# Kernel tuning notes

Hardware: AMD Instinct MI355X
Metric: run time of the kernel (lower is better)

Reference implementation:

```python
import jax, jax.numpy as jnp
import numpy as np

BATCH = 131072
STATE_DIM = 64
CONTROL_DIM = 16
HIDDEN = 256
ALPHA = 0.1
MAX_ITERS = 200
TOL = 0.01
TRACKED_ITERS = 5
U_MIN, U_MAX = -1.0, 1.0


def setup_inputs() -> dict:
    key = jax.random.key(0)
    ks = jax.random.split(key, 8)
    def w(k, shape, fan_in):
        return (jax.random.normal(k, shape, jnp.float32) / np.float32(np.sqrt(fan_in)))
    x = jax.random.normal(ks[0], (BATCH, STATE_DIM), jnp.float32)
    t = jax.random.uniform(ks[1], (1,), jnp.float32)
    W1 = w(ks[2], (STATE_DIM + 1, HIDDEN), STATE_DIM + 1)
    b1 = jnp.zeros((HIDDEN,), jnp.float32)
    W2 = w(ks[3], (HIDDEN, HIDDEN), HIDDEN)
    b2 = jnp.zeros((HIDDEN,), jnp.float32)
    W3 = w(ks[4], (HIDDEN, STATE_DIM), HIDDEN)
    b3 = jnp.zeros((STATE_DIM,), jnp.float32)
    Bmat = w(ks[5], (STATE_DIM, CONTROL_DIM), STATE_DIM)  # oc_problem dynamics matrix
    return {"x": x, "t": t, "W1": W1, "b1": b1, "W2": W2, "b2": b2,
            "W3": W3, "b3": b3, "Bmat": Bmat}


def _p_net(t, x, W1, b1, W2, b2, W3, b3):
    # DefaultPNet: pad x with scalar t, then 3-layer ReLU MLP -> p in [B, state_dim]
    n = x.shape[0]
    tcol = jnp.broadcast_to(t.reshape(1, 1).astype(x.dtype), (n, 1))
    zt = jnp.concatenate([x, tcol], axis=1)
    h = jax.nn.relu(zt @ W1 + b1)
    h = jax.nn.relu(h @ W2 + b2)
    return h @ W3 + b3


def reference(x, t, W1, b1, W2, b2, W3, b3, Bmat):
    # grad_H_u(t,x,u,p) = u + p @ Bmat  (LQ Hamiltonian); p independent of u,
    # so p is computed once (same math as recomputing it every iteration).
    p = _p_net(t, x, W1, b1, W2, b2, W3, b3)          # [B, state_dim]
    pB = p @ Bmat                                      # [B, control_dim]
    clamp = lambda u: jnp.clip(u, U_MIN, U_MAX)
    T = lambda u, pb: u - ALPHA * (u + pb)

    u0 = jnp.zeros((x.shape[0], CONTROL_DIM), x.dtype)
    pB_ng = jax.lax.stop_gradient(pB)

    def cond(st):
        _, i, res = st
        return (res >= TOL) & (i < MAX_ITERS)

    def body(st):
        u, i, _ = st
        u_new = clamp(T(u, pB_ng))
        res = jnp.max(jnp.linalg.norm(u_new - u, axis=1)) / ALPHA
        return (u_new, i + 1, res)

    u_fp, _, _ = jax.lax.while_loop(cond, body, (u0, jnp.int32(0), jnp.float32(jnp.inf)))

    # training path: tracked_iters differentiable refinement steps + final T
    u = jax.lax.stop_gradient(u_fp)
    for _ in range(TRACKED_ITERS + 1):
        u = clamp(T(u, pB))
    return u
```

## Files before the change

kernel.cpp:

```cpp
#include <hip/hip_runtime.h>


typedef __bf16 bf16;
typedef __bf16 bf16x8 __attribute__((ext_vector_type(8)));
typedef __bf16 bf16x4 __attribute__((ext_vector_type(4)));
typedef float  f32x4  __attribute__((ext_vector_type(4)));

#define HID    256
#define SDIM   64
#define CDIM   16
#define BM     64
#define GRID   512
#define ITERS  4

#define OFF_W2P 0
#define OFF_W3P 131072
#define OFF_W1P 139264
#define OFF_B1E 172032
#define OFF_B3B 173056

#define MFMA(a, b, c) __builtin_amdgcn_mfma_f32_16x16x32_bf16(a, b, c, 0, 0, 0)

__device__ __forceinline__ int sh_idx(int row, int h) {
  return (row << 8) + ((((h >> 3) ^ row) & 7) << 3) + (h & 7) + ((h >> 6) << 6);
}
__device__ __forceinline__ int sx_idx(int row, int k) {
  return (row << 6) + ((((k >> 3) ^ row) & 7) << 3) + (k & 7);
}

__global__ __launch_bounds__(512)
void oc_pack(const float* __restrict__ t,  const float* __restrict__ W1,
             const float* __restrict__ b1, const float* __restrict__ W2,
             const float* __restrict__ W3, const float* __restrict__ b3,
             const float* __restrict__ Bmat, char* __restrict__ ws) {
  const int gid = blockIdx.x * 512 + threadIdx.x;
  if (gid < 8192) {
    const int lane = gid & 63, tt = gid >> 6;
    const int nt = tt & 15, kt = tt >> 4;
    const int m = nt * 16 + (lane & 15);
    const int k0 = kt * 32 + ((lane >> 4) << 3);
    bf16x8 v;
#pragma unroll
    for (int j = 0; j < 8; ++j) v[j] = (bf16)W2[(k0 + j) * HID + m];
    *(bf16x8*)((bf16*)(ws + OFF_W2P) + (size_t)gid * 8) = v;
  } else if (gid < 8704) {
    const int e = gid - 8192, kt = e >> 6, fl = e & 63;
    const int r0 = kt * 32 + ((fl >> 4) << 3);
    const int c  = fl & 15;
    float aw[8];
#pragma unroll
    for (int j = 0; j < 8; ++j) aw[j] = 0.f;
    for (int m = 0; m < SDIM; ++m) {
      const float bm = Bmat[m * CDIM + c];
#pragma unroll
      for (int j = 0; j < 8; ++j) aw[j] = fmaf(W3[(r0 + j) * SDIM + m], bm, aw[j]);
    }
    bf16x8 v;
#pragma unroll
    for (int j = 0; j < 8; ++j) v[j] = (bf16)aw[j];
    *(bf16x8*)((bf16*)(ws + OFF_W3P) + (size_t)e * 8) = v;
  } else if (gid < 10752) {
    const int e = gid - 8704;
    const int lane = e & 63, tt = e >> 6;
    const int nt = tt & 15, kt = tt >> 4;
    const int m = nt * 16 + (lane & 15);
    const int k0 = kt * 32 + ((lane >> 4) << 3);
    bf16x8 v;
#pragma unroll
    for (int j = 0; j < 8; ++j) v[j] = (bf16)W1[(k0 + j) * HID + m];
    *(bf16x8*)((bf16*)(ws + OFF_W1P) + (size_t)e * 8) = v;
  } else if (gid < 11008) {
    const int h = gid - 10752;
    ((float*)(ws + OFF_B1E))[h] = b1[h] + t[0] * W1[SDIM * HID + h];
  } else if (gid < 11024) {
    const int c = gid - 11008;
    float s = 0.f;
    for (int m = 0; m < SDIM; ++m) s = fmaf(b3[m], Bmat[m * CDIM + c], s);
    ((float*)(ws + OFF_B3B))[c] = s;
  }
}

__global__ __launch_bounds__(512, 2)
void oc_main(const float* __restrict__ x, const float* __restrict__ b2,
             const char* __restrict__ ws, float* __restrict__ out) {
  __shared__ bf16 sH1[BM * 256];
  __shared__ bf16 sH2[BM * 256];
  __shared__ bf16 sX [BM * 64];
  const int tid  = threadIdx.x;
  const int wave = tid >> 6, lane = tid & 63;
  const int q    = lane >> 4, l = lane & 15;

  const bf16* W2p = (const bf16*)(ws + OFF_W2P);
  const bf16* W3p = (const bf16*)(ws + OFF_W3P);
  const bf16* W1p = (const bf16*)(ws + OFF_W1P);

  {
    const float* xp = x + (size_t)blockIdx.x * BM * SDIM;
#pragma unroll
    for (int i = 0; i < 2; ++i) {
      const int e = i * 512 + tid;
      const int r = e >> 4, k4 = (e & 15) * 4;
      const float4 v = *(const float4*)(xp + r * SDIM + k4);
      bf16x4 w = {(bf16)v.x, (bf16)v.y, (bf16)v.z, (bf16)v.w};
      *(bf16x4*)(&sX[sx_idx(r, k4)]) = w;
    }
  }
  __syncthreads();

  f32x4 acc[2][4];

  for (int it = 0; it < ITERS; ++it) {
    const int tile = blockIdx.x + it * GRID;

#pragma unroll
    for (int mt = 0; mt < 2; ++mt) {
      const float4 v1 = *(const float4*)((const float*)(ws + OFF_B1E) + 32 * wave + 16 * mt + 4 * q);
      const f32x4 bv = {v1.x, v1.y, v1.z, v1.w};
#pragma unroll
      for (int nt = 0; nt < 4; ++nt) acc[mt][nt] = bv;
    }
#pragma unroll
    for (int kt = 0; kt < 2; ++kt) {
      const bf16x8 w1a = *(const bf16x8*)(W1p + ((size_t)(kt * 16 + 2 * wave    ) * 64 + lane) * 8);
      const bf16x8 w1b = *(const bf16x8*)(W1p + ((size_t)(kt * 16 + 2 * wave + 1) * 64 + lane) * 8);
#pragma unroll
      for (int nt = 0; nt < 4; ++nt) {
        const bf16x8 b = *(const bf16x8*)(&sX[sx_idx(16 * nt + l, 32 * kt + 8 * q)]);
        acc[0][nt] = MFMA(w1a, b, acc[0][nt]);
        acc[1][nt] = MFMA(w1b, b, acc[1][nt]);
      }
    }
#pragma unroll
    for (int mt = 0; mt < 2; ++mt) {
      const int h0 = 32 * wave + 16 * mt + 4 * q;
#pragma unroll
      for (int nt = 0; nt < 4; ++nt) {
        bf16x4 v;
#pragma unroll
        for (int r = 0; r < 4; ++r) v[r] = (bf16)fmaxf(acc[mt][nt][r], 0.f);
        *(bf16x4*)(&sH1[sh_idx(16 * nt + l, h0)]) = v;
      }
    }
    __syncthreads();

#pragma unroll
    for (int mt = 0; mt < 2; ++mt) {
      const float4 v2 = *(const float4*)(b2 + 32 * wave + 16 * mt + 4 * q);
      const f32x4 bv = {v2.x, v2.y, v2.z, v2.w};
#pragma unroll
      for (int nt = 0; nt < 4; ++nt) acc[mt][nt] = bv;
    }
#pragma unroll
    for (int kt = 0; kt < 8; ++kt) {
      const bf16x8 w2a = *(const bf16x8*)(W2p + ((size_t)(kt * 16 + 2 * wave    ) * 64 + lane) * 8);
      const bf16x8 w2b = *(const bf16x8*)(W2p + ((size_t)(kt * 16 + 2 * wave + 1) * 64 + lane) * 8);
#pragma unroll
      for (int nt = 0; nt < 4; ++nt) {
        const bf16x8 b = *(const bf16x8*)(&sH1[sh_idx(16 * nt + l, 32 * kt + 8 * q)]);
        acc[0][nt] = MFMA(w2a, b, acc[0][nt]);
        acc[1][nt] = MFMA(w2b, b, acc[1][nt]);
      }
    }
    __syncthreads();

#pragma unroll
    for (int mt = 0; mt < 2; ++mt) {
      const int h0 = 32 * wave + 16 * mt + 4 * q;
#pragma unroll
      for (int nt = 0; nt < 4; ++nt) {
        bf16x4 hi, lo;
#pragma unroll
        for (int r = 0; r < 4; ++r) {
          const float v = fmaxf(acc[mt][nt][r], 0.f);
          const bf16 h = (bf16)v;
          hi[r] = h;
          lo[r] = (bf16)(v - (float)h);
        }
        const int idx = sh_idx(16 * nt + l, h0);
        *(bf16x4*)(&sH2[idx]) = hi;
        *(bf16x4*)(&sH1[idx]) = lo;
      }
    }
    __syncthreads();

    if (wave < 4) {
      const float4 v3 = *(const float4*)((const float*)(ws + OFF_B3B) + 4 * q);
      f32x4 a3 = {v3.x, v3.y, v3.z, v3.w};
      const int row = 16 * wave + l;
#pragma unroll
      for (int kt = 0; kt < 8; ++kt) {
        const bf16x8 w3 = *(const bf16x8*)(W3p + ((size_t)kt * 64 + lane) * 8);
        const int idx = sh_idx(row, 32 * kt + 8 * q);
        const bf16x8 bh = *(const bf16x8*)(&sH2[idx]);
        const bf16x8 bl = *(const bf16x8*)(&sH1[idx]);
        a3 = MFMA(w3, bh, a3);
        a3 = MFMA(w3, bl, a3);
      }
      f32x4 o;
#pragma unroll
      for (int r = 0; r < 4; ++r)
        o[r] = fminf(fmaxf(-a3[r], -1.f), 1.f);
      *(float4*)(&out[((size_t)tile * BM + row) * CDIM + 4 * q]) = *(float4*)&o;
    } else if (it + 1 < ITERS) {
      const float* xp = x + (size_t)(tile + GRID) * BM * SDIM;
      const int tid2 = tid - 256;
#pragma unroll
      for (int i = 0; i < 4; ++i) {
        const int e = i * 256 + tid2;
        const int r = e >> 4, k4 = (e & 15) * 4;
        const float4 v = *(const float4*)(xp + r * SDIM + k4);
        bf16x4 w = {(bf16)v.x, (bf16)v.y, (bf16)v.z, (bf16)v.w};
        *(bf16x4*)(&sX[sx_idx(r, k4)]) = w;
      }
    }
    __syncthreads();
  }
}

extern "C" void kernel_launch(void* const* d_in, const int* in_sizes, int n_in,
                              void* d_out, int out_size, void* d_ws, size_t ws_size,
                              hipStream_t stream) {
  const float* x    = (const float*)d_in[0];
  const float* t    = (const float*)d_in[1];
  const float* W1   = (const float*)d_in[2];
  const float* b1   = (const float*)d_in[3];
  const float* W2   = (const float*)d_in[4];
  const float* b2   = (const float*)d_in[5];
  const float* W3   = (const float*)d_in[6];
  const float* b3   = (const float*)d_in[7];
  const float* Bmat = (const float*)d_in[8];
  float* out = (float*)d_out;
  char*  ws  = (char*)d_ws;

  hipLaunchKernelGGL(oc_pack, dim3(22), dim3(512), 0, stream,
                     t, W1, b1, W2, W3, b3, Bmat, ws);
  hipLaunchKernelGGL(oc_main, dim3(GRID), dim3(512), 0, stream,
                     x, b2, ws, out);
}
```

Measured before the change: 126.4 us.

## Double row tile to 128 with 1024-thread blocks sharing weight fragments

Each block now handles 128 rows with 16 waves. Waves are split into 8 hidden-column groups and 2 row halves, so one set of W1/W2 register fragments is spread across more rows per block. The grid is halved to 256 blocks, and the W2 and W3 loops drop to unroll-by-2, presumably to limit register pressure at 1024 threads. LDS per block doubles to about 144KB, which likely allows only one block per CU. The grid now covers fewer CUs than the device has (256 blocks).

```diff
diff --git a/kernel.cpp b/kernel.cpp
--- a/kernel.cpp
+++ b/kernel.cpp
@@ -9,8 +9,8 @@
 #define HID    256
 #define SDIM   64
 #define CDIM   16
-#define BM     64
-#define GRID   512
+#define BM     128
+#define GRID   256
 #define ITERS  4
 
 #define OFF_W2P 0
@@ -80,7 +80,7 @@
   }
 }
 
-__global__ __launch_bounds__(512, 2)
+__global__ __launch_bounds__(1024)
 void oc_main(const float* __restrict__ x, const float* __restrict__ b2,
              const char* __restrict__ ws, float* __restrict__ out) {
   __shared__ bf16 sH1[BM * 256];
@@ -89,6 +89,8 @@
   const int tid  = threadIdx.x;
   const int wave = tid >> 6, lane = tid & 63;
   const int q    = lane >> 4, l = lane & 15;
+  const int mg   = wave >> 1;
+  const int ng   = wave & 1;
 
   const bf16* W2p = (const bf16*)(ws + OFF_W2P);
   const bf16* W3p = (const bf16*)(ws + OFF_W3P);
@@ -98,7 +100,7 @@
     const float* xp = x + (size_t)blockIdx.x * BM * SDIM;
 #pragma unroll
     for (int i = 0; i < 2; ++i) {
-      const int e = i * 512 + tid;
+      const int e = i * 1024 + tid;
       const int r = e >> 4, k4 = (e & 15) * 4;
       const float4 v = *(const float4*)(xp + r * SDIM + k4);
       bf16x4 w = {(bf16)v.x, (bf16)v.y, (bf16)v.z, (bf16)v.w};
@@ -114,49 +116,49 @@
 
 #pragma unroll
     for (int mt = 0; mt < 2; ++mt) {
-      const float4 v1 = *(const float4*)((const float*)(ws + OFF_B1E) + 32 * wave + 16 * mt + 4 * q);
+      const float4 v1 = *(const float4*)((const float*)(ws + OFF_B1E) + 32 * mg + 16 * mt + 4 * q);
       const f32x4 bv = {v1.x, v1.y, v1.z, v1.w};
 #pragma unroll
       for (int nt = 0; nt < 4; ++nt) acc[mt][nt] = bv;
     }
 #pragma unroll
     for (int kt = 0; kt < 2; ++kt) {
-      const bf16x8 w1a = *(const bf16x8*)(W1p + ((size_t)(kt * 16 + 2 * wave    ) * 64 + lane) * 8);
-      const bf16x8 w1b = *(const bf16x8*)(W1p + ((size_t)(kt * 16 + 2 * wave + 1) * 64 + lane) * 8);
-#pragma unroll
-      for (int nt = 0; nt < 4; ++nt) {
-        const bf16x8 b = *(const bf16x8*)(&sX[sx_idx(16 * nt + l, 32 * kt + 8 * q)]);
+      const bf16x8 w1a = *(const bf16x8*)(W1p + ((size_t)(kt * 16 + 2 * mg    ) * 64 + lane) * 8);
+      const bf16x8 w1b = *(const bf16x8*)(W1p + ((size_t)(kt * 16 + 2 * mg + 1) * 64 + lane) * 8);
+#pragma unroll
+      for (int nt = 0; nt < 4; ++nt) {
+        const bf16x8 b = *(const bf16x8*)(&sX[sx_idx(64 * ng + 16 * nt + l, 32 * kt + 8 * q)]);
         acc[0][nt] = MFMA(w1a, b, acc[0][nt]);
         acc[1][nt] = MFMA(w1b, b, acc[1][nt]);
       }
     }
 #pragma unroll
     for (int mt = 0; mt < 2; ++mt) {
-      const int h0 = 32 * wave + 16 * mt + 4 * q;
+      const int h0 = 32 * mg + 16 * mt + 4 * q;
 #pragma unroll
       for (int nt = 0; nt < 4; ++nt) {
         bf16x4 v;
 #pragma unroll
         for (int r = 0; r < 4; ++r) v[r] = (bf16)fmaxf(acc[mt][nt][r], 0.f);
-        *(bf16x4*)(&sH1[sh_idx(16 * nt + l, h0)]) = v;
-      }
-    }
-    __syncthreads();
-
-#pragma unroll
-    for (int mt = 0; mt < 2; ++mt) {
-      const float4 v2 = *(const float4*)(b2 + 32 * wave + 16 * mt + 4 * q);
+        *(bf16x4*)(&sH1[sh_idx(64 * ng + 16 * nt + l, h0)]) = v;
+      }
+    }
+    __syncthreads();
+
+#pragma unroll
+    for (int mt = 0; mt < 2; ++mt) {
+      const float4 v2 = *(const float4*)(b2 + 32 * mg + 16 * mt + 4 * q);
       const f32x4 bv = {v2.x, v2.y, v2.z, v2.w};
 #pragma unroll
       for (int nt = 0; nt < 4; ++nt) acc[mt][nt] = bv;
     }
-#pragma unroll
+#pragma unroll 2
     for (int kt = 0; kt < 8; ++kt) {
-      const bf16x8 w2a = *(const bf16x8*)(W2p + ((size_t)(kt * 16 + 2 * wave    ) * 64 + lane) * 8);
-      const bf16x8 w2b = *(const bf16x8*)(W2p + ((size_t)(kt * 16 + 2 * wave + 1) * 64 + lane) * 8);
-#pragma unroll
-      for (int nt = 0; nt < 4; ++nt) {
-        const bf16x8 b = *(const bf16x8*)(&sH1[sh_idx(16 * nt + l, 32 * kt + 8 * q)]);
+      const bf16x8 w2a = *(const bf16x8*)(W2p + ((size_t)(kt * 16 + 2 * mg    ) * 64 + lane) * 8);
+      const bf16x8 w2b = *(const bf16x8*)(W2p + ((size_t)(kt * 16 + 2 * mg + 1) * 64 + lane) * 8);
+#pragma unroll
+      for (int nt = 0; nt < 4; ++nt) {
+        const bf16x8 b = *(const bf16x8*)(&sH1[sh_idx(64 * ng + 16 * nt + l, 32 * kt + 8 * q)]);
         acc[0][nt] = MFMA(w2a, b, acc[0][nt]);
         acc[1][nt] = MFMA(w2b, b, acc[1][nt]);
       }
@@ -165,7 +167,7 @@
 
 #pragma unroll
     for (int mt = 0; mt < 2; ++mt) {
-      const int h0 = 32 * wave + 16 * mt + 4 * q;
+      const int h0 = 32 * mg + 16 * mt + 4 * q;
 #pragma unroll
       for (int nt = 0; nt < 4; ++nt) {
         bf16x4 hi, lo;
@@ -176,18 +178,18 @@
           hi[r] = h;
           lo[r] = (bf16)(v - (float)h);
         }
-        const int idx = sh_idx(16 * nt + l, h0);
+        const int idx = sh_idx(64 * ng + 16 * nt + l, h0);
         *(bf16x4*)(&sH2[idx]) = hi;
         *(bf16x4*)(&sH1[idx]) = lo;
       }
     }
     __syncthreads();
 
-    if (wave < 4) {
+    if (wave < 8) {
       const float4 v3 = *(const float4*)((const float*)(ws + OFF_B3B) + 4 * q);
       f32x4 a3 = {v3.x, v3.y, v3.z, v3.w};
       const int row = 16 * wave + l;
-#pragma unroll
+#pragma unroll 2
       for (int kt = 0; kt < 8; ++kt) {
         const bf16x8 w3 = *(const bf16x8*)(W3p + ((size_t)kt * 64 + lane) * 8);
         const int idx = sh_idx(row, 32 * kt + 8 * q);
@@ -203,10 +205,10 @@
       *(float4*)(&out[((size_t)tile * BM + row) * CDIM + 4 * q]) = *(float4*)&o;
     } else if (it + 1 < ITERS) {
       const float* xp = x + (size_t)(tile + GRID) * BM * SDIM;
-      const int tid2 = tid - 256;
+      const int tid2 = tid - 512;
 #pragma unroll
       for (int i = 0; i < 4; ++i) {
-        const int e = i * 256 + tid2;
+        const int e = i * 512 + tid2;
         const int r = e >> 4, k4 = (e & 15) * 4;
         const float4 v = *(const float4*)(xp + r * SDIM + k4);
         bf16x4 w = {(bf16)v.x, (bf16)v.y, (bf16)v.z, (bf16)v.w};
@@ -234,6 +236,6 @@
 
   hipLaunchKernelGGL(oc_pack, dim3(22), dim3(512), 0, stream,
                      t, W1, b1, W2, W3, b3, Bmat, ws);
-  hipLaunchKernelGGL(oc_main, dim3(GRID), dim3(512), 0, stream,
+  hipLaunchKernelGGL(oc_main, dim3(GRID), dim3(1024), 0, stream,
                      x, b2, ws, out);
 }
```

Result: slower. 130.4 us (+3.2%).
